# Kernel tuning notes

Measured on AMD Instinct MI355X. Metric: run time of the kernel, lower is better.

The kernel has to match this reference:

```python
import jax, jax.numpy as jnp
from jax import lax
import numpy as np

I, H, O, B, T = 8, 64, 8, 256, 2048


def setup_inputs() -> dict:
    key = jax.random.key(0)
    ks = jax.random.split(key, 12)
    s_ih = 1.0 / np.sqrt(H)
    u = lambda k, shape: jax.random.uniform(k, shape, jnp.float32, -s_ih, s_ih)
    return {
        "x": jax.random.normal(ks[0], (B, T, I), jnp.float32),
        "W_ih0": u(ks[1], (H, I)),
        "W_hh0": u(ks[2], (H, H)),
        "b_ih0": u(ks[3], (H,)),
        "b_hh0": u(ks[4], (H,)),
        "W_ih1": u(ks[5], (H, H)),
        "W_hh1": u(ks[6], (H, H)),
        "b_ih1": u(ks[7], (H,)),
        "b_hh1": u(ks[8], (H,)),
        "W_fc": u(ks[9], (O, H)),
        "b_fc": u(ks[10], (O,)),
    }


def reference(x, W_ih0, W_hh0, b_ih0, b_hh0, W_ih1, W_hh1, b_ih1, b_hh1, W_fc, b_fc):
    Bx = x.shape[0]
    xt = jnp.swapaxes(x, 0, 1)  # [T, B, I]
    h_init = (jnp.zeros((Bx, H), x.dtype), jnp.zeros((Bx, H), x.dtype))

    def step(carry, x_t):
        h0, h1 = carry
        h0n = jnp.tanh(x_t @ W_ih0.T + b_ih0 + h0 @ W_hh0.T + b_hh0)
        h1n = jnp.tanh(h0n @ W_ih1.T + b_ih1 + h1 @ W_hh1.T + b_hh1)
        return (h0n, h1n), h1n

    (h0f, h1f), outs = lax.scan(step, h_init, xt)  # outs: [T, B, H]
    out = jnp.swapaxes(outs, 0, 1).reshape(-1, H) @ W_fc.T + b_fc  # [B*T, O]
    hidden = jnp.stack([h0f, h1f])  # [2, B, H]
    return out, hidden
```

## Files before the change

kernel.cpp:

```cpp
#include <hip/hip_runtime.h>

#define NI 8
#define NH 64
#define NO 8
#define NB 256
#define NT 2048

typedef float v2f __attribute__((ext_vector_type(2)));

__device__ __forceinline__ v2f fma2(v2f a, v2f b, v2f c) {
    return __builtin_elementwise_fma(a, b, c);
}

__device__ __forceinline__ float tanh_fast(float s) {
    float e = __expf(2.0f * s);
    return fmaf(-2.0f, __builtin_amdgcn_rcpf(e + 1.0f), 1.0f);
}

__attribute__((amdgpu_waves_per_eu(1, 1)))
__global__ void __launch_bounds__(192) rnn_tri4(
    const float* __restrict__ x,
    const float* __restrict__ W_ih0, const float* __restrict__ W_hh0,
    const float* __restrict__ b_ih0, const float* __restrict__ b_hh0,
    const float* __restrict__ W_ih1, const float* __restrict__ W_hh1,
    const float* __restrict__ b_ih1, const float* __restrict__ b_hh1,
    const float* __restrict__ W_fc,  const float* __restrict__ b_fc,
    float* __restrict__ out)
{
    const int b    = blockIdx.x;
    const int tid  = threadIdx.x;
    const int wid  = tid >> 6;
    const int lane = tid & 63;

    __shared__ __align__(16) float ur[32][NH];
    __shared__ __align__(16) float pir[32][NH];
    __shared__ __align__(16) float h0s[NH];
    __shared__ __align__(16) float h1s[NH];
    __shared__ int fa, fc2, fu;

    if (tid == 0) { fa = -1; fc2 = -1; fu = -1; }
    __syncthreads();

    volatile int* vfa  = &fa;
    volatile int* vfc2 = &fc2;
    volatile int* vfu  = &fu;

    const float*  xb   = x   + (size_t)b * NT * NI;
    float*        outb = out + (size_t)b * NT * NO;
    const size_t  hid  = (size_t)NB * NT * NO;

    if (wid == 0) {
        v2f wh[NH / 2], wi[NH / 2];
        #pragma unroll
        for (int k = 0; k < NH / 2; ++k) {
            wh[k] = v2f{W_hh0[lane * NH + 2 * k], W_hh0[lane * NH + 2 * k + 1]};
            wi[k] = v2f{W_ih1[lane * NH + 2 * k], W_ih1[lane * NH + 2 * k + 1]};
        }
        float h0n = 0.0f, dI_prev = 0.0f;

        while (*vfu < 7) {}
        asm volatile("" ::: "memory");
        float uv_next = ur[0][lane];

        for (int t = 0; t < NT; ++t) {
            if ((t & 7) == 0) {
                const int needU = (t + 8 < NT) ? t + 8 : NT - 1;
                while (*vfu < needU) {}
                while (*vfc2 < t - 27) {}
                asm volatile("" ::: "memory");
            }
            h0s[lane] = h0n;
            const float4* hp = (const float4*)h0s;
            float4 gv[16];
            #pragma unroll
            for (int k = 0; k < 16; ++k) gv[k] = hp[k];
            if (t >= 2) pir[(t - 2) & 31][lane] = dI_prev;
            const float uv_cur = uv_next;
            uv_next = ur[(t + 1) & 31][lane];

            v2f aW0 = {0,0}, aW1 = {0,0}, aW2 = {0,0}, aW3 = {0,0};
            v2f aI0 = {0,0}, aI1 = {0,0}, aI2 = {0,0}, aI3 = {0,0};
            #pragma unroll
            for (int k = 0; k < 16; ++k) {
                const v2f lo = {gv[k].x, gv[k].y}, hi = {gv[k].z, gv[k].w};
                if (k & 1) {
                    aW2 = fma2(lo, wh[2 * k], aW2); aW3 = fma2(hi, wh[2 * k + 1], aW3);
                    aI2 = fma2(lo, wi[2 * k], aI2); aI3 = fma2(hi, wi[2 * k + 1], aI3);
                } else {
                    aW0 = fma2(lo, wh[2 * k], aW0); aW1 = fma2(hi, wh[2 * k + 1], aW1);
                    aI0 = fma2(lo, wi[2 * k], aI0); aI1 = fma2(hi, wi[2 * k + 1], aI1);
                }
            }
            if (t & 1) {
                asm volatile("s_waitcnt lgkmcnt(0)" ::: "memory");
                *vfa = t - 2;
            }
            const v2f sW = (aW0 + aW1) + (aW2 + aW3);
            const v2f sI = (aI0 + aI1) + (aI2 + aI3);
            dI_prev = sI.x + sI.y;
            h0n = tanh_fast(sW.x + sW.y + uv_cur);
        }

        while (*vfc2 < NT - 33) {}
        asm volatile("" ::: "memory");
        pir[(NT - 2) & 31][lane] = dI_prev;
        h0s[lane] = h0n;
        {
            const float4* hp = (const float4*)h0s;
            v2f aI0 = {0,0}, aI1 = {0,0}, aI2 = {0,0}, aI3 = {0,0};
            #pragma unroll
            for (int k = 0; k < 16; ++k) {
                const float4 g = hp[k];
                const v2f lo = {g.x, g.y}, hi = {g.z, g.w};
                if (k & 1) { aI2 = fma2(lo, wi[2 * k], aI2); aI3 = fma2(hi, wi[2 * k + 1], aI3); }
                else       { aI0 = fma2(lo, wi[2 * k], aI0); aI1 = fma2(hi, wi[2 * k + 1], aI1); }
            }
            const v2f sI = (aI0 + aI1) + (aI2 + aI3);
            pir[(NT - 1) & 31][lane] = sI.x + sI.y;
        }
        asm volatile("s_waitcnt lgkmcnt(0)" ::: "memory");
        *vfa = NT - 1;
        out[hid + (size_t)b * NH + lane] = h0n;
    } else if (wid == 1) {
        const int o = lane & 7;
        v2f wh1[NH / 2], wf[NH / 2];
        #pragma unroll
        for (int k = 0; k < NH / 2; ++k) {
            wh1[k] = v2f{W_hh1[lane * NH + 2 * k], W_hh1[lane * NH + 2 * k + 1]};
            wf[k]  = v2f{W_fc[o * NH + 2 * k],     W_fc[o * NH + 2 * k + 1]};
        }
        const float bias1 = b_ih1[lane] + b_hh1[lane];
        const float bfc   = b_fc[o];
        float h1n = 0.0f;

        while (*vfa < 1) {}
        asm volatile("" ::: "memory");
        float pv_next = pir[0][lane];

        for (int t = 0; t < NT; ++t) {
            if ((t & 3) == 0) {
                const int need = (t + 4 < NT) ? t + 4 : NT - 1;
                while (*vfa < need) {}
                asm volatile("" ::: "memory");
            }
            h1s[lane] = h1n;
            const float4* hp = (const float4*)h1s;
            float4 gv[16];
            #pragma unroll
            for (int k = 0; k < 16; ++k) gv[k] = hp[k];
            const float pv_cur = pv_next;
            pv_next = pir[(t + 1) & 31][lane];

            v2f aW0 = {0,0}, aW1 = {0,0}, aW2 = {0,0}, aW3 = {0,0};
            #pragma unroll
            for (int k = 0; k < 16; ++k) {
                const v2f lo = {gv[k].x, gv[k].y}, hi = {gv[k].z, gv[k].w};
                if (k & 1) { aW2 = fma2(lo, wh1[2 * k], aW2); aW3 = fma2(hi, wh1[2 * k + 1], aW3); }
                else       { aW0 = fma2(lo, wh1[2 * k], aW0); aW1 = fma2(hi, wh1[2 * k + 1], aW1); }
            }
            const v2f sW = (aW0 + aW1) + (aW2 + aW3);
            h1n = tanh_fast(sW.x + sW.y + pv_cur + bias1);

            v2f aF0 = {0,0}, aF1 = {0,0}, aF2 = {0,0}, aF3 = {0,0};
            #pragma unroll
            for (int k = 0; k < 16; ++k) {
                const v2f lo = {gv[k].x, gv[k].y}, hi = {gv[k].z, gv[k].w};
                if (k & 1) { aF2 = fma2(lo, wf[2 * k], aF2); aF3 = fma2(hi, wf[2 * k + 1], aF3); }
                else       { aF0 = fma2(lo, wf[2 * k], aF0); aF1 = fma2(hi, wf[2 * k + 1], aF1); }
            }
            const v2f sF = (aF0 + aF1) + (aF2 + aF3);
            if (t > 0 && lane < NO)
                outb[(size_t)(t - 1) * NO + o] = sF.x + sF.y + bfc;

            if ((t & 3) == 3) {
                asm volatile("s_waitcnt lgkmcnt(0)" ::: "memory");
                *vfc2 = t;
            }
        }

        h1s[lane] = h1n;
        {
            const float4* hp = (const float4*)h1s;
            v2f aF0 = {0,0}, aF1 = {0,0}, aF2 = {0,0}, aF3 = {0,0};
            #pragma unroll
            for (int k = 0; k < 16; ++k) {
                const float4 g = hp[k];
                const v2f lo = {g.x, g.y}, hi = {g.z, g.w};
                if (k & 1) { aF2 = fma2(lo, wf[2 * k], aF2); aF3 = fma2(hi, wf[2 * k + 1], aF3); }
                else       { aF0 = fma2(lo, wf[2 * k], aF0); aF1 = fma2(hi, wf[2 * k + 1], aF1); }
            }
            const v2f sF = (aF0 + aF1) + (aF2 + aF3);
            if (lane < NO) outb[(size_t)(NT - 1) * NO + o] = sF.x + sF.y + bfc;
        }
        out[hid + (size_t)NB * NH + (size_t)b * NH + lane] = h1n;
    } else if (wid == 2) {
        float wih0r[NI];
        #pragma unroll
        for (int i = 0; i < NI; ++i) wih0r[i] = W_ih0[lane * NI + i];
        const float bias0 = b_ih0[lane] + b_hh0[lane];

        float4 xc[16], xn[16];
        #pragma unroll
        for (int j = 0; j < 8; ++j) {
            xc[2 * j]     = *(const float4*)(xb + (size_t)j * NI);
            xc[2 * j + 1] = *(const float4*)(xb + (size_t)j * NI + 4);
        }
        #pragma unroll
        for (int j = 0; j < 8; ++j) {
            xn[2 * j]     = *(const float4*)(xb + (size_t)(8 + j) * NI);
            xn[2 * j + 1] = *(const float4*)(xb + (size_t)(8 + j) * NI + 4);
        }

        for (int w = 0; w < NT / 8; ++w) {
            while (*vfa < 8 * w - 20) {}
            asm volatile("" ::: "memory");
            #pragma unroll
            for (int j = 0; j < 8; ++j) {
                float u = bias0;
                u = fmaf(xc[2 * j].x,     wih0r[0], u);
                u = fmaf(xc[2 * j].y,     wih0r[1], u);
                u = fmaf(xc[2 * j].z,     wih0r[2], u);
                u = fmaf(xc[2 * j].w,     wih0r[3], u);
                u = fmaf(xc[2 * j + 1].x, wih0r[4], u);
                u = fmaf(xc[2 * j + 1].y, wih0r[5], u);
                u = fmaf(xc[2 * j + 1].z, wih0r[6], u);
                u = fmaf(xc[2 * j + 1].w, wih0r[7], u);
                ur[(8 * w + j) & 31][lane] = u;
            }
            asm volatile("s_waitcnt lgkmcnt(0)" ::: "memory");
            *vfu = 8 * w + 7;
            #pragma unroll
            for (int j = 0; j < 16; ++j) xc[j] = xn[j];
            if (w + 2 < NT / 8) {
                const size_t base = (size_t)(w + 2) * 8;
                #pragma unroll
                for (int j = 0; j < 8; ++j) {
                    xn[2 * j]     = *(const float4*)(xb + (base + j) * NI);
                    xn[2 * j + 1] = *(const float4*)(xb + (base + j) * NI + 4);
                }
            }
        }
    }
}

extern "C" void kernel_launch(void* const* d_in, const int* in_sizes, int n_in,
                              void* d_out, int out_size, void* d_ws, size_t ws_size,
                              hipStream_t stream) {
    const float* x     = (const float*)d_in[0];
    const float* W_ih0 = (const float*)d_in[1];
    const float* W_hh0 = (const float*)d_in[2];
    const float* b_ih0 = (const float*)d_in[3];
    const float* b_hh0 = (const float*)d_in[4];
    const float* W_ih1 = (const float*)d_in[5];
    const float* W_hh1 = (const float*)d_in[6];
    const float* b_ih1 = (const float*)d_in[7];
    const float* b_hh1 = (const float*)d_in[8];
    const float* W_fc  = (const float*)d_in[9];
    const float* b_fc  = (const float*)d_in[10];

    rnn_tri4<<<dim3(NB), dim3(192), 0, stream>>>(
        x, W_ih0, W_hh0, b_ih0, b_hh0,
        W_ih1, W_hh1, b_ih1, b_hh1, W_fc, b_fc,
        (float*)d_out);
}
```

Before: 710.7 us.

## Process two batch sequences per block to interleave independent recurrences

```diff
diff --git a/kernel.cpp b/kernel.cpp
--- a/kernel.cpp
+++ b/kernel.cpp
@@ -5,6 +5,7 @@
 #define NO 8
 #define NB 256
 #define NT 2048
+#define NBLK (NB / 2)
 
 typedef float v2f __attribute__((ext_vector_type(2)));
 
@@ -18,7 +19,7 @@
 }
 
 __attribute__((amdgpu_waves_per_eu(1, 1)))
-__global__ void __launch_bounds__(192) rnn_tri4(
+__global__ void __launch_bounds__(192) rnn_dual(
     const float* __restrict__ x,
     const float* __restrict__ W_ih0, const float* __restrict__ W_hh0,
     const float* __restrict__ b_ih0, const float* __restrict__ b_hh0,
@@ -27,15 +28,16 @@
     const float* __restrict__ W_fc,  const float* __restrict__ b_fc,
     float* __restrict__ out)
 {
-    const int b    = blockIdx.x;
+    const int blk  = blockIdx.x;
+    const int b0   = 2 * blk, b1 = 2 * blk + 1;
     const int tid  = threadIdx.x;
     const int wid  = tid >> 6;
     const int lane = tid & 63;
 
-    __shared__ __align__(16) float ur[32][NH];
-    __shared__ __align__(16) float pir[32][NH];
-    __shared__ __align__(16) float h0s[NH];
-    __shared__ __align__(16) float h1s[NH];
+    __shared__ __align__(16) float ur[2][32][NH];
+    __shared__ __align__(16) float pir[2][32][NH];
+    __shared__ __align__(16) float h0s[2][NH];
+    __shared__ __align__(16) float h1s[2][NH];
     __shared__ int fa, fc2, fu;
 
     if (tid == 0) { fa = -1; fc2 = -1; fu = -1; }
@@ -45,9 +47,11 @@
     volatile int* vfc2 = &fc2;
     volatile int* vfu  = &fu;
 
-    const float*  xb   = x   + (size_t)b * NT * NI;
-    float*        outb = out + (size_t)b * NT * NO;
-    const size_t  hid  = (size_t)NB * NT * NO;
+    const float* xb0   = x + (size_t)b0 * NT * NI;
+    const float* xb1   = x + (size_t)b1 * NT * NI;
+    float*       outb0 = out + (size_t)b0 * NT * NO;
+    float*       outb1 = out + (size_t)b1 * NT * NO;
+    const size_t hid   = (size_t)NB * NT * NO;
 
     if (wid == 0) {
         v2f wh[NH / 2], wi[NH / 2];
@@ -56,11 +60,14 @@
             wh[k] = v2f{W_hh0[lane * NH + 2 * k], W_hh0[lane * NH + 2 * k + 1]};
             wi[k] = v2f{W_ih1[lane * NH + 2 * k], W_ih1[lane * NH + 2 * k + 1]};
         }
-        float h0n = 0.0f, dI_prev = 0.0f;
-
-        while (*vfu < 7) {}
+        #pragma unroll
+        for (int k = 0; k < NH / 2; ++k) { asm("" : "+v"(wh[k])); asm("" : "+v"(wi[k])); }
+
+        float h0n0 = 0.0f, h0n1 = 0.0f, dI0 = 0.0f, dI1 = 0.0f;
+
+        while (*vfu < 11) {}
         asm volatile("" ::: "memory");
-        float uv_next = ur[0][lane];
+        float uv0n = ur[0][0][lane], uv1n = ur[1][0][lane];
 
         for (int t = 0; t < NT; ++t) {
             if ((t & 7) == 0) {
@@ -69,58 +76,88 @@
                 while (*vfc2 < t - 27) {}
                 asm volatile("" ::: "memory");
             }
-            h0s[lane] = h0n;
-            const float4* hp = (const float4*)h0s;
-            float4 gv[16];
-            #pragma unroll
-            for (int k = 0; k < 16; ++k) gv[k] = hp[k];
-            if (t >= 2) pir[(t - 2) & 31][lane] = dI_prev;
-            const float uv_cur = uv_next;
-            uv_next = ur[(t + 1) & 31][lane];
-
-            v2f aW0 = {0,0}, aW1 = {0,0}, aW2 = {0,0}, aW3 = {0,0};
-            v2f aI0 = {0,0}, aI1 = {0,0}, aI2 = {0,0}, aI3 = {0,0};
+            h0s[0][lane] = h0n0;
+            h0s[1][lane] = h0n1;
+            if (t >= 2) {
+                pir[0][(t - 2) & 31][lane] = dI0;
+                pir[1][(t - 2) & 31][lane] = dI1;
+            }
+            const float uv0c = uv0n, uv1c = uv1n;
+            uv0n = ur[0][(t + 1) & 31][lane];
+            uv1n = ur[1][(t + 1) & 31][lane];
+
+            const float4* hp0 = (const float4*)&h0s[0][0];
+            const float4* hp1 = (const float4*)&h0s[1][0];
+            v2f W0a={0,0},W0b={0,0},W0c={0,0},W0d={0,0};
+            v2f I0a={0,0},I0b={0,0},I0c={0,0},I0d={0,0};
+            v2f W1a={0,0},W1b={0,0},W1c={0,0},W1d={0,0};
+            v2f I1a={0,0},I1b={0,0},I1c={0,0},I1d={0,0};
             #pragma unroll
             for (int k = 0; k < 16; ++k) {
-                const v2f lo = {gv[k].x, gv[k].y}, hi = {gv[k].z, gv[k].w};
+                const float4 g0 = hp0[k];
+                const float4 g1 = hp1[k];
+                const v2f l0 = {g0.x, g0.y}, u0 = {g0.z, g0.w};
+                const v2f l1 = {g1.x, g1.y}, u1 = {g1.z, g1.w};
                 if (k & 1) {
-                    aW2 = fma2(lo, wh[2 * k], aW2); aW3 = fma2(hi, wh[2 * k + 1], aW3);
-                    aI2 = fma2(lo, wi[2 * k], aI2); aI3 = fma2(hi, wi[2 * k + 1], aI3);
+                    W0c = fma2(l0, wh[2*k], W0c); W0d = fma2(u0, wh[2*k+1], W0d);
+                    I0c = fma2(l0, wi[2*k], I0c); I0d = fma2(u0, wi[2*k+1], I0d);
+                    W1c = fma2(l1, wh[2*k], W1c); W1d = fma2(u1, wh[2*k+1], W1d);
+                    I1c = fma2(l1, wi[2*k], I1c); I1d = fma2(u1, wi[2*k+1], I1d);
                 } else {
-                    aW0 = fma2(lo, wh[2 * k], aW0); aW1 = fma2(hi, wh[2 * k + 1], aW1);
-                    aI0 = fma2(lo, wi[2 * k], aI0); aI1 = fma2(hi, wi[2 * k + 1], aI1);
+                    W0a = fma2(l0, wh[2*k], W0a); W0b = fma2(u0, wh[2*k+1], W0b);
+                    I0a = fma2(l0, wi[2*k], I0a); I0b = fma2(u0, wi[2*k+1], I0b);
+                    W1a = fma2(l1, wh[2*k], W1a); W1b = fma2(u1, wh[2*k+1], W1b);
+                    I1a = fma2(l1, wi[2*k], I1a); I1b = fma2(u1, wi[2*k+1], I1b);
                 }
             }
             if (t & 1) {
                 asm volatile("s_waitcnt lgkmcnt(0)" ::: "memory");
                 *vfa = t - 2;
             }
-            const v2f sW = (aW0 + aW1) + (aW2 + aW3);
-            const v2f sI = (aI0 + aI1) + (aI2 + aI3);
-            dI_prev = sI.x + sI.y;
-            h0n = tanh_fast(sW.x + sW.y + uv_cur);
+            const v2f sW0 = (W0a + W0b) + (W0c + W0d);
+            const v2f sI0 = (I0a + I0b) + (I0c + I0d);
+            const v2f sW1 = (W1a + W1b) + (W1c + W1d);
+            const v2f sI1 = (I1a + I1b) + (I1c + I1d);
+            dI0 = sI0.x + sI0.y;
+            dI1 = sI1.x + sI1.y;
+            h0n0 = tanh_fast(sW0.x + sW0.y + uv0c);
+            h0n1 = tanh_fast(sW1.x + sW1.y + uv1c);
         }
 
         while (*vfc2 < NT - 33) {}
         asm volatile("" ::: "memory");
-        pir[(NT - 2) & 31][lane] = dI_prev;
-        h0s[lane] = h0n;
+        pir[0][(NT - 2) & 31][lane] = dI0;
+        pir[1][(NT - 2) & 31][lane] = dI1;
+        h0s[0][lane] = h0n0;
+        h0s[1][lane] = h0n1;
         {
-            const float4* hp = (const float4*)h0s;
-            v2f aI0 = {0,0}, aI1 = {0,0}, aI2 = {0,0}, aI3 = {0,0};
+            const float4* hp0 = (const float4*)&h0s[0][0];
+            const float4* hp1 = (const float4*)&h0s[1][0];
+            v2f I0a={0,0},I0b={0,0},I0c={0,0},I0d={0,0};
+            v2f I1a={0,0},I1b={0,0},I1c={0,0},I1d={0,0};
             #pragma unroll
             for (int k = 0; k < 16; ++k) {
-                const float4 g = hp[k];
-                const v2f lo = {g.x, g.y}, hi = {g.z, g.w};
-                if (k & 1) { aI2 = fma2(lo, wi[2 * k], aI2); aI3 = fma2(hi, wi[2 * k + 1], aI3); }
-                else       { aI0 = fma2(lo, wi[2 * k], aI0); aI1 = fma2(hi, wi[2 * k + 1], aI1); }
-            }
-            const v2f sI = (aI0 + aI1) + (aI2 + aI3);
-            pir[(NT - 1) & 31][lane] = sI.x + sI.y;
+                const float4 g0 = hp0[k];
+                const float4 g1 = hp1[k];
+                const v2f l0 = {g0.x, g0.y}, u0 = {g0.z, g0.w};
+                const v2f l1 = {g1.x, g1.y}, u1 = {g1.z, g1.w};
+                if (k & 1) {
+                    I0c = fma2(l0, wi[2*k], I0c); I0d = fma2(u0, wi[2*k+1], I0d);
+                    I1c = fma2(l1, wi[2*k], I1c); I1d = fma2(u1, wi[2*k+1], I1d);
+                } else {
+                    I0a = fma2(l0, wi[2*k], I0a); I0b = fma2(u0, wi[2*k+1], I0b);
+                    I1a = fma2(l1, wi[2*k], I1a); I1b = fma2(u1, wi[2*k+1], I1b);
+                }
+            }
+            const v2f sI0 = (I0a + I0b) + (I0c + I0d);
+            const v2f sI1 = (I1a + I1b) + (I1c + I1d);
+            pir[0][(NT - 1) & 31][lane] = sI0.x + sI0.y;
+            pir[1][(NT - 1) & 31][lane] = sI1.x + sI1.y;
         }
         asm volatile("s_waitcnt lgkmcnt(0)" ::: "memory");
         *vfa = NT - 1;
-        out[hid + (size_t)b * NH + lane] = h0n;
+        out[hid + (size_t)b0 * NH + lane] = h0n0;
+        out[hid + (size_t)b1 * NH + lane] = h0n1;
     } else if (wid == 1) {
         const int o = lane & 7;
         v2f wh1[NH / 2], wf[NH / 2];
@@ -129,13 +166,15 @@
             wh1[k] = v2f{W_hh1[lane * NH + 2 * k], W_hh1[lane * NH + 2 * k + 1]};
             wf[k]  = v2f{W_fc[o * NH + 2 * k],     W_fc[o * NH + 2 * k + 1]};
         }
+        #pragma unroll
+        for (int k = 0; k < NH / 2; ++k) { asm("" : "+v"(wh1[k])); asm("" : "+v"(wf[k])); }
         const float bias1 = b_ih1[lane] + b_hh1[lane];
         const float bfc   = b_fc[o];
-        float h1n = 0.0f;
+        float h1n0 = 0.0f, h1n1 = 0.0f;
 
         while (*vfa < 1) {}
         asm volatile("" ::: "memory");
-        float pv_next = pir[0][lane];
+        float pv0n = pir[0][0][lane], pv1n = pir[1][0][lane];
 
         for (int t = 0; t < NT; ++t) {
             if ((t & 3) == 0) {
@@ -143,100 +182,156 @@
                 while (*vfa < need) {}
                 asm volatile("" ::: "memory");
             }
-            h1s[lane] = h1n;
-            const float4* hp = (const float4*)h1s;
-            float4 gv[16];
-            #pragma unroll
-            for (int k = 0; k < 16; ++k) gv[k] = hp[k];
-            const float pv_cur = pv_next;
-            pv_next = pir[(t + 1) & 31][lane];
-
-            v2f aW0 = {0,0}, aW1 = {0,0}, aW2 = {0,0}, aW3 = {0,0};
+            h1s[0][lane] = h1n0;
+            h1s[1][lane] = h1n1;
+            const float pv0c = pv0n, pv1c = pv1n;
+            pv0n = pir[0][(t + 1) & 31][lane];
+            pv1n = pir[1][(t + 1) & 31][lane];
+
+            const float4* hp0 = (const float4*)&h1s[0][0];
+            const float4* hp1 = (const float4*)&h1s[1][0];
+            v2f W0a={0,0},W0b={0,0},W0c={0,0},W0d={0,0};
+            v2f F0a={0,0},F0b={0,0},F0c={0,0},F0d={0,0};
+            v2f W1a={0,0},W1b={0,0},W1c={0,0},W1d={0,0};
+            v2f F1a={0,0},F1b={0,0},F1c={0,0},F1d={0,0};
             #pragma unroll
             for (int k = 0; k < 16; ++k) {
-                const v2f lo = {gv[k].x, gv[k].y}, hi = {gv[k].z, gv[k].w};
-                if (k & 1) { aW2 = fma2(lo, wh1[2 * k], aW2); aW3 = fma2(hi, wh1[2 * k + 1], aW3); }
-                else       { aW0 = fma2(lo, wh1[2 * k], aW0); aW1 = fma2(hi, wh1[2 * k + 1], aW1); }
-            }
-            const v2f sW = (aW0 + aW1) + (aW2 + aW3);
-            h1n = tanh_fast(sW.x + sW.y + pv_cur + bias1);
-
-            v2f aF0 = {0,0}, aF1 = {0,0}, aF2 = {0,0}, aF3 = {0,0};
-            #pragma unroll
-            for (int k = 0; k < 16; ++k) {
-                const v2f lo = {gv[k].x, gv[k].y}, hi = {gv[k].z, gv[k].w};
-                if (k & 1) { aF2 = fma2(lo, wf[2 * k], aF2); aF3 = fma2(hi, wf[2 * k + 1], aF3); }
-                else       { aF0 = fma2(lo, wf[2 * k], aF0); aF1 = fma2(hi, wf[2 * k + 1], aF1); }
-            }
-            const v2f sF = (aF0 + aF1) + (aF2 + aF3);
-            if (t > 0 && lane < NO)
-                outb[(size_t)(t - 1) * NO + o] = sF.x + sF.y + bfc;
-
+                const float4 g0 = hp0[k];
+                const float4 g1 = hp1[k];
+                const v2f l0 = {g0.x, g0.y}, u0 = {g0.z, g0.w};
+                const v2f l1 = {g1.x, g1.y}, u1 = {g1.z, g1.w};
+                if (k & 1) {
+                    W0c = fma2(l0, wh1[2*k], W0c); W0d = fma2(u0, wh1[2*k+1], W0d);
+                    F0c = fma2(l0, wf[2*k],  F0c); F0d = fma2(u0, wf[2*k+1],  F0d);
+                    W1c = fma2(l1, wh1[2*k], W1c); W1d = fma2(u1, wh1[2*k+1], W1d);
+                    F1c = fma2(l1, wf[2*k],  F1c); F1d = fma2(u1, wf[2*k+1],  F1d);
+                } else {
+                    W0a = fma2(l0, wh1[2*k], W0a); W0b = fma2(u0, wh1[2*k+1], W0b);
+                    F0a = fma2(l0, wf[2*k],  F0a); F0b = fma2(u0, wf[2*k+1],  F0b);
+                    W1a = fma2(l1, wh1[2*k], W1a); W1b = fma2(u1, wh1[2*k+1], W1b);
+                    F1a = fma2(l1, wf[2*k],  F1a); F1b = fma2(u1, wf[2*k+1],  F1b);
+                }
+            }
+            const v2f sW0 = (W0a + W0b) + (W0c + W0d);
+            const v2f sF0 = (F0a + F0b) + (F0c + F0d);
+            const v2f sW1 = (W1a + W1b) + (W1c + W1d);
+            const v2f sF1 = (F1a + F1b) + (F1c + F1d);
+            if (t > 0) {
+                if (lane < NO)
+                    outb0[(size_t)(t - 1) * NO + o] = sF0.x + sF0.y + bfc;
+                else if (lane < 2 * NO)
+                    outb1[(size_t)(t - 1) * NO + o] = sF1.x + sF1.y + bfc;
+            }
+            h1n0 = tanh_fast(sW0.x + sW0.y + pv0c + bias1);
+            h1n1 = tanh_fast(sW1.x + sW1.y + pv1c + bias1);
             if ((t & 3) == 3) {
                 asm volatile("s_waitcnt lgkmcnt(0)" ::: "memory");
                 *vfc2 = t;
             }
         }
 
-        h1s[lane] = h1n;
+        h1s[0][lane] = h1n0;
+        h1s[1][lane] = h1n1;
         {
-            const float4* hp = (const float4*)h1s;
-            v2f aF0 = {0,0}, aF1 = {0,0}, aF2 = {0,0}, aF3 = {0,0};
+            const float4* hp0 = (const float4*)&h1s[0][0];
+            const float4* hp1 = (const float4*)&h1s[1][0];
+            v2f F0a={0,0},F0b={0,0},F0c={0,0},F0d={0,0};
+            v2f F1a={0,0},F1b={0,0},F1c={0,0},F1d={0,0};
             #pragma unroll
             for (int k = 0; k < 16; ++k) {
-                const float4 g = hp[k];
-                const v2f lo = {g.x, g.y}, hi = {g.z, g.w};
-                if (k & 1) { aF2 = fma2(lo, wf[2 * k], aF2); aF3 = fma2(hi, wf[2 * k + 1], aF3); }
-                else       { aF0 = fma2(lo, wf[2 * k], aF0); aF1 = fma2(hi, wf[2 * k + 1], aF1); }
-            }
-            const v2f sF = (aF0 + aF1) + (aF2 + aF3);
-            if (lane < NO) outb[(size_t)(NT - 1) * NO + o] = sF.x + sF.y + bfc;
-        }
-        out[hid + (size_t)NB * NH + (size_t)b * NH + lane] = h1n;
+                const float4 g0 = hp0[k];
+                const float4 g1 = hp1[k];
+                const v2f l0 = {g0.x, g0.y}, u0 = {g0.z, g0.w};
+                const v2f l1 = {g1.x, g1.y}, u1 = {g1.z, g1.w};
+                if (k & 1) {
+                    F0c = fma2(l0, wf[2*k], F0c); F0d = fma2(u0, wf[2*k+1], F0d);
+                    F1c = fma2(l1, wf[2*k], F1c); F1d = fma2(u1, wf[2*k+1], F1d);
+                } else {
+                    F0a = fma2(l0, wf[2*k], F0a); F0b = fma2(u0, wf[2*k+1], F0b);
+                    F1a = fma2(l1, wf[2*k], F1a); F1b = fma2(u1, wf[2*k+1], F1b);
+                }
+            }
+            const v2f sF0 = (F0a + F0b) + (F0c + F0d);
+            const v2f sF1 = (F1a + F1b) + (F1c + F1d);
+            if (lane < NO)
+                outb0[(size_t)(NT - 1) * NO + o] = sF0.x + sF0.y + bfc;
+            else if (lane < 2 * NO)
+                outb1[(size_t)(NT - 1) * NO + o] = sF1.x + sF1.y + bfc;
+        }
+        out[hid + (size_t)NB * NH + (size_t)b0 * NH + lane] = h1n0;
+        out[hid + (size_t)NB * NH + (size_t)b1 * NH + lane] = h1n1;
     } else if (wid == 2) {
         float wih0r[NI];
         #pragma unroll
         for (int i = 0; i < NI; ++i) wih0r[i] = W_ih0[lane * NI + i];
         const float bias0 = b_ih0[lane] + b_hh0[lane];
 
-        float4 xc[16], xn[16];
-        #pragma unroll
-        for (int j = 0; j < 8; ++j) {
-            xc[2 * j]     = *(const float4*)(xb + (size_t)j * NI);
-            xc[2 * j + 1] = *(const float4*)(xb + (size_t)j * NI + 4);
-        }
-        #pragma unroll
-        for (int j = 0; j < 8; ++j) {
-            xn[2 * j]     = *(const float4*)(xb + (size_t)(8 + j) * NI);
-            xn[2 * j + 1] = *(const float4*)(xb + (size_t)(8 + j) * NI + 4);
-        }
-
-        for (int w = 0; w < NT / 8; ++w) {
-            while (*vfa < 8 * w - 20) {}
+        #pragma unroll
+        for (int s = 0; s < 12; ++s) {
+            const float4 a0 = *(const float4*)(xb0 + (size_t)s * NI);
+            const float4 a1 = *(const float4*)(xb0 + (size_t)s * NI + 4);
+            const float4 c0 = *(const float4*)(xb1 + (size_t)s * NI);
+            const float4 c1 = *(const float4*)(xb1 + (size_t)s * NI + 4);
+            float u0 = bias0, u1 = bias0;
+            u0 = fmaf(a0.x, wih0r[0], u0); u0 = fmaf(a0.y, wih0r[1], u0);
+            u0 = fmaf(a0.z, wih0r[2], u0); u0 = fmaf(a0.w, wih0r[3], u0);
+            u0 = fmaf(a1.x, wih0r[4], u0); u0 = fmaf(a1.y, wih0r[5], u0);
+            u0 = fmaf(a1.z, wih0r[6], u0); u0 = fmaf(a1.w, wih0r[7], u0);
+            u1 = fmaf(c0.x, wih0r[0], u1); u1 = fmaf(c0.y, wih0r[1], u1);
+            u1 = fmaf(c0.z, wih0r[2], u1); u1 = fmaf(c0.w, wih0r[3], u1);
+            u1 = fmaf(c1.x, wih0r[4], u1); u1 = fmaf(c1.y, wih0r[5], u1);
+            u1 = fmaf(c1.z, wih0r[6], u1); u1 = fmaf(c1.w, wih0r[7], u1);
+            ur[0][s][lane] = u0;
+            ur[1][s][lane] = u1;
+        }
+        asm volatile("s_waitcnt lgkmcnt(0)" ::: "memory");
+        *vfu = 11;
+
+        float4 xc0[8], xc1[8], xn0[8], xn1[8];
+        #pragma unroll
+        for (int j = 0; j < 4; ++j) {
+            xc0[2*j]   = *(const float4*)(xb0 + (size_t)(12 + j) * NI);
+            xc0[2*j+1] = *(const float4*)(xb0 + (size_t)(12 + j) * NI + 4);
+            xc1[2*j]   = *(const float4*)(xb1 + (size_t)(12 + j) * NI);
+            xc1[2*j+1] = *(const float4*)(xb1 + (size_t)(12 + j) * NI + 4);
+        }
+        #pragma unroll
+        for (int j = 0; j < 4; ++j) {
+            xn0[2*j]   = *(const float4*)(xb0 + (size_t)(16 + j) * NI);
+            xn0[2*j+1] = *(const float4*)(xb0 + (size_t)(16 + j) * NI + 4);
+            xn1[2*j]   = *(const float4*)(xb1 + (size_t)(16 + j) * NI);
+            xn1[2*j+1] = *(const float4*)(xb1 + (size_t)(16 + j) * NI + 4);
+        }
+
+        for (int w = 3; w < NT / 4; ++w) {
+            while (*vfa < 4 * w - 20) {}
             asm volatile("" ::: "memory");
             #pragma unroll
-            for (int j = 0; j < 8; ++j) {
-                float u = bias0;
-                u = fmaf(xc[2 * j].x,     wih0r[0], u);
-                u = fmaf(xc[2 * j].y,     wih0r[1], u);
-                u = fmaf(xc[2 * j].z,     wih0r[2], u);
-                u = fmaf(xc[2 * j].w,     wih0r[3], u);
-                u = fmaf(xc[2 * j + 1].x, wih0r[4], u);
-                u = fmaf(xc[2 * j + 1].y, wih0r[5], u);
-                u = fmaf(xc[2 * j + 1].z, wih0r[6], u);
-                u = fmaf(xc[2 * j + 1].w, wih0r[7], u);
-                ur[(8 * w + j) & 31][lane] = u;
+            for (int j = 0; j < 4; ++j) {
+                float u0 = bias0, u1 = bias0;
+                u0 = fmaf(xc0[2*j].x,   wih0r[0], u0); u0 = fmaf(xc0[2*j].y,   wih0r[1], u0);
+                u0 = fmaf(xc0[2*j].z,   wih0r[2], u0); u0 = fmaf(xc0[2*j].w,   wih0r[3], u0);
+                u0 = fmaf(xc0[2*j+1].x, wih0r[4], u0); u0 = fmaf(xc0[2*j+1].y, wih0r[5], u0);
+                u0 = fmaf(xc0[2*j+1].z, wih0r[6], u0); u0 = fmaf(xc0[2*j+1].w, wih0r[7], u0);
+                u1 = fmaf(xc1[2*j].x,   wih0r[0], u1); u1 = fmaf(xc1[2*j].y,   wih0r[1], u1);
+                u1 = fmaf(xc1[2*j].z,   wih0r[2], u1); u1 = fmaf(xc1[2*j].w,   wih0r[3], u1);
+                u1 = fmaf(xc1[2*j+1].x, wih0r[4], u1); u1 = fmaf(xc1[2*j+1].y, wih0r[5], u1);
+                u1 = fmaf(xc1[2*j+1].z, wih0r[6], u1); u1 = fmaf(xc1[2*j+1].w, wih0r[7], u1);
+                ur[0][(4 * w + j) & 31][lane] = u0;
+                ur[1][(4 * w + j) & 31][lane] = u1;
             }
             asm volatile("s_waitcnt lgkmcnt(0)" ::: "memory");
-            *vfu = 8 * w + 7;
-            #pragma unroll
-            for (int j = 0; j < 16; ++j) xc[j] = xn[j];
-            if (w + 2 < NT / 8) {
-                const size_t base = (size_t)(w + 2) * 8;
+            *vfu = 4 * w + 3;
+            #pragma unroll
+            for (int j = 0; j < 8; ++j) { xc0[j] = xn0[j]; xc1[j] = xn1[j]; }
+            if (w + 2 < NT / 4) {
+                const size_t base = (size_t)(w + 2) * 4;
                 #pragma unroll
-                for (int j = 0; j < 8; ++j) {
-                    xn[2 * j]     = *(const float4*)(xb + (base + j) * NI);
-                    xn[2 * j + 1] = *(const float4*)(xb + (base + j) * NI + 4);
+                for (int j = 0; j < 4; ++j) {
+                    xn0[2*j]   = *(const float4*)(xb0 + (base + j) * NI);
+                    xn0[2*j+1] = *(const float4*)(xb0 + (base + j) * NI + 4);
+                    xn1[2*j]   = *(const float4*)(xb1 + (base + j) * NI);
+                    xn1[2*j+1] = *(const float4*)(xb1 + (base + j) * NI + 4);
                 }
             }
         }
@@ -258,7 +353,7 @@
     const float* W_fc  = (const float*)d_in[9];
     const float* b_fc  = (const float*)d_in[10];
 
-    rnn_tri4<<<dim3(NB), dim3(192), 0, stream>>>(
+    rnn_dual<<<dim3(NBLK), dim3(192), 0, stream>>>(
         x, W_ih0, W_hh0, b_ih0, b_hh0,
         W_ih1, W_hh1, b_ih1, b_hh1, W_fc, b_fc,
         (float*)d_out);
```

Result: slower. 1.433 ms (+101.6%).

## Fold input projection into layer-0 wave and drop the third producer wave

Applied to the files above, without the earlier changes.

```diff
diff --git a/kernel.cpp b/kernel.cpp
--- a/kernel.cpp
+++ b/kernel.cpp
@@ -18,7 +18,7 @@
 }
 
 __attribute__((amdgpu_waves_per_eu(1, 1)))
-__global__ void __launch_bounds__(192) rnn_tri4(
+__global__ void __launch_bounds__(128) rnn_duo2(
     const float* __restrict__ x,
     const float* __restrict__ W_ih0, const float* __restrict__ W_hh0,
     const float* __restrict__ b_ih0, const float* __restrict__ b_hh0,
@@ -31,66 +31,86 @@
     const int tid  = threadIdx.x;
     const int wid  = tid >> 6;
     const int lane = tid & 63;
-
-    __shared__ __align__(16) float ur[32][NH];
+    const int o    = lane & 7;
+
+    __shared__ __align__(16) float xs[2][64][NI];
     __shared__ __align__(16) float pir[32][NH];
     __shared__ __align__(16) float h0s[NH];
     __shared__ __align__(16) float h1s[NH];
-    __shared__ int fa, fc2, fu;
-
-    if (tid == 0) { fa = -1; fc2 = -1; fu = -1; }
+    __shared__ int fa, fc2;
+
+    if (tid == 0) { fa = -1; fc2 = -1; }
     __syncthreads();
 
     volatile int* vfa  = &fa;
     volatile int* vfc2 = &fc2;
-    volatile int* vfu  = &fu;
 
     const float*  xb   = x   + (size_t)b * NT * NI;
     float*        outb = out + (size_t)b * NT * NO;
     const size_t  hid  = (size_t)NB * NT * NO;
 
     if (wid == 0) {
-        v2f wh[NH / 2], wi[NH / 2];
+        v2f wh[NH / 2], wi[NH / 2], wx[NI / 2];
         #pragma unroll
         for (int k = 0; k < NH / 2; ++k) {
             wh[k] = v2f{W_hh0[lane * NH + 2 * k], W_hh0[lane * NH + 2 * k + 1]};
             wi[k] = v2f{W_ih1[lane * NH + 2 * k], W_ih1[lane * NH + 2 * k + 1]};
         }
+        #pragma unroll
+        for (int m = 0; m < NI / 2; ++m)
+            wx[m] = v2f{W_ih0[lane * NI + 2 * m], W_ih0[lane * NI + 2 * m + 1]};
+        #pragma unroll
+        for (int k = 0; k < NH / 2; ++k) { asm("" : "+v"(wh[k])); asm("" : "+v"(wi[k])); }
+        const float bias0 = b_ih0[lane] + b_hh0[lane];
+
+        {
+            float4 q0 = *(const float4*)(xb + (size_t)lane * NI);
+            float4 q1 = *(const float4*)(xb + (size_t)lane * NI + 4);
+            *(float4*)(&xs[0][lane][0]) = q0;
+            *(float4*)(&xs[0][lane][4]) = q1;
+        }
+        float4 xn0 = {0, 0, 0, 0}, xn1 = {0, 0, 0, 0};
         float h0n = 0.0f, dI_prev = 0.0f;
 
-        while (*vfu < 7) {}
-        asm volatile("" ::: "memory");
-        float uv_next = ur[0][lane];
-
         for (int t = 0; t < NT; ++t) {
+            const int m  = t & 63;
+            const int cb = (t >> 6) & 1;
+            if (m == 0) {
+                const int c = (t >> 6) + 1;
+                if (c < NT / 64) {
+                    xn0 = *(const float4*)(xb + (size_t)(c * 64 + lane) * NI);
+                    xn1 = *(const float4*)(xb + (size_t)(c * 64 + lane) * NI + 4);
+                }
+            }
             if ((t & 7) == 0) {
-                const int needU = (t + 8 < NT) ? t + 8 : NT - 1;
-                while (*vfu < needU) {}
                 while (*vfc2 < t - 27) {}
                 asm volatile("" ::: "memory");
             }
             h0s[lane] = h0n;
             const float4* hp = (const float4*)h0s;
-            float4 gv[16];
-            #pragma unroll
-            for (int k = 0; k < 16; ++k) gv[k] = hp[k];
+            const float4  xv0 = ((const float4*)&xs[cb][m][0])[0];
+            const float4  xv1 = ((const float4*)&xs[cb][m][0])[1];
             if (t >= 2) pir[(t - 2) & 31][lane] = dI_prev;
-            const float uv_cur = uv_next;
-            uv_next = ur[(t + 1) & 31][lane];
-
-            v2f aW0 = {0,0}, aW1 = {0,0}, aW2 = {0,0}, aW3 = {0,0};
+
+            v2f aW0 = {bias0, 0.f}, aW1 = {0,0}, aW2 = {0,0}, aW3 = {0,0};
             v2f aI0 = {0,0}, aI1 = {0,0}, aI2 = {0,0}, aI3 = {0,0};
             #pragma unroll
             for (int k = 0; k < 16; ++k) {
-                const v2f lo = {gv[k].x, gv[k].y}, hi = {gv[k].z, gv[k].w};
+                const float4 g = hp[k];
+                const v2f lo = {g.x, g.y}, hi = {g.z, g.w};
                 if (k & 1) {
-                    aW2 = fma2(lo, wh[2 * k], aW2); aW3 = fma2(hi, wh[2 * k + 1], aW3);
-                    aI2 = fma2(lo, wi[2 * k], aI2); aI3 = fma2(hi, wi[2 * k + 1], aI3);
+                    aW2 = fma2(lo, wh[2*k], aW2); aW3 = fma2(hi, wh[2*k+1], aW3);
+                    aI2 = fma2(lo, wi[2*k], aI2); aI3 = fma2(hi, wi[2*k+1], aI3);
                 } else {
-                    aW0 = fma2(lo, wh[2 * k], aW0); aW1 = fma2(hi, wh[2 * k + 1], aW1);
-                    aI0 = fma2(lo, wi[2 * k], aI0); aI1 = fma2(hi, wi[2 * k + 1], aI1);
-                }
-            }
+                    aW0 = fma2(lo, wh[2*k], aW0); aW1 = fma2(hi, wh[2*k+1], aW1);
+                    aI0 = fma2(lo, wi[2*k], aI0); aI1 = fma2(hi, wi[2*k+1], aI1);
+                }
+            }
+            aW0 = fma2(v2f{xv0.x, xv0.y}, wx[0], aW0);
+            aW1 = fma2(v2f{xv0.z, xv0.w}, wx[1], aW1);
+            aW2 = fma2(v2f{xv1.x, xv1.y}, wx[2], aW2);
+            aW3 = fma2(v2f{xv1.z, xv1.w}, wx[3], aW3);
+
             if (t & 1) {
                 asm volatile("s_waitcnt lgkmcnt(0)" ::: "memory");
                 *vfa = t - 2;
@@ -98,10 +118,18 @@
             const v2f sW = (aW0 + aW1) + (aW2 + aW3);
             const v2f sI = (aI0 + aI1) + (aI2 + aI3);
             dI_prev = sI.x + sI.y;
-            h0n = tanh_fast(sW.x + sW.y + uv_cur);
-        }
-
-        while (*vfc2 < NT - 33) {}
+            h0n = tanh_fast(sW.x + sW.y);
+
+            if (m == 32) {
+                const int c = (t >> 6) + 1;
+                if (c < NT / 64) {
+                    *(float4*)(&xs[cb ^ 1][lane][0]) = xn0;
+                    *(float4*)(&xs[cb ^ 1][lane][4]) = xn1;
+                }
+            }
+        }
+
+        while (*vfc2 < NT - 29) {}
         asm volatile("" ::: "memory");
         pir[(NT - 2) & 31][lane] = dI_prev;
         h0s[lane] = h0n;
@@ -112,8 +140,8 @@
             for (int k = 0; k < 16; ++k) {
                 const float4 g = hp[k];
                 const v2f lo = {g.x, g.y}, hi = {g.z, g.w};
-                if (k & 1) { aI2 = fma2(lo, wi[2 * k], aI2); aI3 = fma2(hi, wi[2 * k + 1], aI3); }
-                else       { aI0 = fma2(lo, wi[2 * k], aI0); aI1 = fma2(hi, wi[2 * k + 1], aI1); }
+                if (k & 1) { aI2 = fma2(lo, wi[2*k], aI2); aI3 = fma2(hi, wi[2*k+1], aI3); }
+                else       { aI0 = fma2(lo, wi[2*k], aI0); aI1 = fma2(hi, wi[2*k+1], aI1); }
             }
             const v2f sI = (aI0 + aI1) + (aI2 + aI3);
             pir[(NT - 1) & 31][lane] = sI.x + sI.y;
@@ -121,19 +149,20 @@
         asm volatile("s_waitcnt lgkmcnt(0)" ::: "memory");
         *vfa = NT - 1;
         out[hid + (size_t)b * NH + lane] = h0n;
-    } else if (wid == 1) {
-        const int o = lane & 7;
+    } else {
         v2f wh1[NH / 2], wf[NH / 2];
         #pragma unroll
         for (int k = 0; k < NH / 2; ++k) {
             wh1[k] = v2f{W_hh1[lane * NH + 2 * k], W_hh1[lane * NH + 2 * k + 1]};
             wf[k]  = v2f{W_fc[o * NH + 2 * k],     W_fc[o * NH + 2 * k + 1]};
         }
+        #pragma unroll
+        for (int k = 0; k < NH / 2; ++k) { asm("" : "+v"(wh1[k])); asm("" : "+v"(wf[k])); }
         const float bias1 = b_ih1[lane] + b_hh1[lane];
         const float bfc   = b_fc[o];
         float h1n = 0.0f;
 
-        while (*vfa < 1) {}
+        while (*vfa < 0) {}
         asm volatile("" ::: "memory");
         float pv_next = pir[0][lane];
 
@@ -143,35 +172,32 @@
                 while (*vfa < need) {}
                 asm volatile("" ::: "memory");
             }
+            const float pv_cur = pv_next;
+            pv_next = pir[(t + 1) & 31][lane];
+
             h1s[lane] = h1n;
             const float4* hp = (const float4*)h1s;
-            float4 gv[16];
-            #pragma unroll
-            for (int k = 0; k < 16; ++k) gv[k] = hp[k];
-            const float pv_cur = pv_next;
-            pv_next = pir[(t + 1) & 31][lane];
-
-            v2f aW0 = {0,0}, aW1 = {0,0}, aW2 = {0,0}, aW3 = {0,0};
-            #pragma unroll
-            for (int k = 0; k < 16; ++k) {
-                const v2f lo = {gv[k].x, gv[k].y}, hi = {gv[k].z, gv[k].w};
-                if (k & 1) { aW2 = fma2(lo, wh1[2 * k], aW2); aW3 = fma2(hi, wh1[2 * k + 1], aW3); }
-                else       { aW0 = fma2(lo, wh1[2 * k], aW0); aW1 = fma2(hi, wh1[2 * k + 1], aW1); }
-            }
-            const v2f sW = (aW0 + aW1) + (aW2 + aW3);
-            h1n = tanh_fast(sW.x + sW.y + pv_cur + bias1);
-
+            v2f aH0 = {bias1, 0.f}, aH1 = {0,0}, aH2 = {0,0}, aH3 = {0,0};
             v2f aF0 = {0,0}, aF1 = {0,0}, aF2 = {0,0}, aF3 = {0,0};
             #pragma unroll
             for (int k = 0; k < 16; ++k) {
-                const v2f lo = {gv[k].x, gv[k].y}, hi = {gv[k].z, gv[k].w};
-                if (k & 1) { aF2 = fma2(lo, wf[2 * k], aF2); aF3 = fma2(hi, wf[2 * k + 1], aF3); }
-                else       { aF0 = fma2(lo, wf[2 * k], aF0); aF1 = fma2(hi, wf[2 * k + 1], aF1); }
-            }
+                const float4 g = hp[k];
+                const v2f lo = {g.x, g.y}, hi = {g.z, g.w};
+                if (k & 1) {
+                    aH2 = fma2(lo, wh1[2*k], aH2); aH3 = fma2(hi, wh1[2*k+1], aH3);
+                    aF2 = fma2(lo, wf[2*k],  aF2); aF3 = fma2(hi, wf[2*k+1],  aF3);
+                } else {
+                    aH0 = fma2(lo, wh1[2*k], aH0); aH1 = fma2(hi, wh1[2*k+1], aH1);
+                    aF0 = fma2(lo, wf[2*k],  aF0); aF1 = fma2(hi, wf[2*k+1],  aF1);
+                }
+            }
+            const v2f sH = (aH0 + aH1) + (aH2 + aH3);
             const v2f sF = (aF0 + aF1) + (aF2 + aF3);
+
             if (t > 0 && lane < NO)
                 outb[(size_t)(t - 1) * NO + o] = sF.x + sF.y + bfc;
 
+            h1n = tanh_fast(sH.x + sH.y + pv_cur);
             if ((t & 3) == 3) {
                 asm volatile("s_waitcnt lgkmcnt(0)" ::: "memory");
                 *vfc2 = t;
@@ -186,60 +212,13 @@
             for (int k = 0; k < 16; ++k) {
                 const float4 g = hp[k];
                 const v2f lo = {g.x, g.y}, hi = {g.z, g.w};
-                if (k & 1) { aF2 = fma2(lo, wf[2 * k], aF2); aF3 = fma2(hi, wf[2 * k + 1], aF3); }
-                else       { aF0 = fma2(lo, wf[2 * k], aF0); aF1 = fma2(hi, wf[2 * k + 1], aF1); }
+                if (k & 1) { aF2 = fma2(lo, wf[2*k], aF2); aF3 = fma2(hi, wf[2*k+1], aF3); }
+                else       { aF0 = fma2(lo, wf[2*k], aF0); aF1 = fma2(hi, wf[2*k+1], aF1); }
             }
             const v2f sF = (aF0 + aF1) + (aF2 + aF3);
             if (lane < NO) outb[(size_t)(NT - 1) * NO + o] = sF.x + sF.y + bfc;
         }
         out[hid + (size_t)NB * NH + (size_t)b * NH + lane] = h1n;
-    } else if (wid == 2) {
-        float wih0r[NI];
-        #pragma unroll
-        for (int i = 0; i < NI; ++i) wih0r[i] = W_ih0[lane * NI + i];
-        const float bias0 = b_ih0[lane] + b_hh0[lane];
-
-        float4 xc[16], xn[16];
-        #pragma unroll
-        for (int j = 0; j < 8; ++j) {
-            xc[2 * j]     = *(const float4*)(xb + (size_t)j * NI);
-            xc[2 * j + 1] = *(const float4*)(xb + (size_t)j * NI + 4);
-        }
-        #pragma unroll
-        for (int j = 0; j < 8; ++j) {
-            xn[2 * j]     = *(const float4*)(xb + (size_t)(8 + j) * NI);
-            xn[2 * j + 1] = *(const float4*)(xb + (size_t)(8 + j) * NI + 4);
-        }
-
-        for (int w = 0; w < NT / 8; ++w) {
-            while (*vfa < 8 * w - 20) {}
-            asm volatile("" ::: "memory");
-            #pragma unroll
-            for (int j = 0; j < 8; ++j) {
-                float u = bias0;
-                u = fmaf(xc[2 * j].x,     wih0r[0], u);
-                u = fmaf(xc[2 * j].y,     wih0r[1], u);
-                u = fmaf(xc[2 * j].z,     wih0r[2], u);
-                u = fmaf(xc[2 * j].w,     wih0r[3], u);
-                u = fmaf(xc[2 * j + 1].x, wih0r[4], u);
-                u = fmaf(xc[2 * j + 1].y, wih0r[5], u);
-                u = fmaf(xc[2 * j + 1].z, wih0r[6], u);
-                u = fmaf(xc[2 * j + 1].w, wih0r[7], u);
-                ur[(8 * w + j) & 31][lane] = u;
-            }
-            asm volatile("s_waitcnt lgkmcnt(0)" ::: "memory");
-            *vfu = 8 * w + 7;
-            #pragma unroll
-            for (int j = 0; j < 16; ++j) xc[j] = xn[j];
-            if (w + 2 < NT / 8) {
-                const size_t base = (size_t)(w + 2) * 8;
-                #pragma unroll
-                for (int j = 0; j < 8; ++j) {
-                    xn[2 * j]     = *(const float4*)(xb + (base + j) * NI);
-                    xn[2 * j + 1] = *(const float4*)(xb + (base + j) * NI + 4);
-                }
-            }
-        }
     }
 }
 
@@ -258,7 +237,7 @@
     const float* W_fc  = (const float*)d_in[9];
     const float* b_fc  = (const float*)d_in[10];
 
-    rnn_tri4<<<dim3(NB), dim3(192), 0, stream>>>(
+    rnn_duo2<<<dim3(NB), dim3(128), 0, stream>>>(
         x, W_ih0, W_hh0, b_ih0, b_hh0,
         W_ih1, W_hh1, b_ih1, b_hh1, W_fc, b_fc,
         (float*)d_out);
```

Result: slower. 787.1 us (+10.7%).
